# Performance work log

Hardware: AMD Instinct MI355X
Metric: run time of the kernel (lower is better)

The kernel has to match this reference:

```python
import jax, jax.numpy as jnp
import numpy as np

NEG = -1.0e9  # large negative number used for causal masking in the original


def setup_inputs() -> dict:
    key = jax.random.key(0)
    ks = jax.random.split(key, 9)
    B, S, D, H = 4, 4096, 512, 64
    sd = 1.0 / np.sqrt(D)
    sh = 1.0 / np.sqrt(H)
    return {
        "x": jax.random.normal(ks[0], (B, S, D), jnp.float32),
        # nn.Linear(d_model, d_head): stored here as (in, out) matrices
        "Wq": jax.random.normal(ks[1], (D, H), jnp.float32) * sd,
        "bq": jax.random.normal(ks[2], (H,), jnp.float32) * 0.01,
        "Wk": jax.random.normal(ks[3], (D, H), jnp.float32) * sd,
        "bk": jax.random.normal(ks[4], (H,), jnp.float32) * 0.01,
        "Wv": jax.random.normal(ks[5], (D, H), jnp.float32) * sd,
        "bv": jax.random.normal(ks[6], (H,), jnp.float32) * 0.01,
        "Wo": jax.random.normal(ks[7], (H, D), jnp.float32) * sh,
        "bo": jax.random.normal(ks[8], (D,), jnp.float32) * 0.01,
    }


def reference(x, Wq, bq, Wk, bk, Wv, bv, Wo, bo):
    # x: (B, S, D)
    B, S, D = x.shape
    Q = x @ Wq + bq  # (B, S, H)
    K = x @ Wk + bk
    V = x @ Wv + bv
    scores = jnp.einsum("bsh,bth->bst", Q, K)  # (B, S, S)
    # NOTE: original divides by sqrt(scores.shape[-1]) == sqrt(seq_len), not sqrt(d_head)
    scores = scores / jnp.sqrt(jnp.asarray(S, scores.dtype))
    # causal mask: strictly-upper-triangular entries get NEG added
    mask = jnp.triu(jnp.full((S, S), NEG, dtype=scores.dtype), k=1)
    attn = jax.nn.softmax(scores + mask[None, :, :], axis=-1)
    out = jnp.einsum("bst,bth->bsh", attn, V)  # (B, S, H)
    return out @ Wo + bo  # (B, S, D)
```

## Files before the change

### kernel.cpp

```cpp
#include <hip/hip_runtime.h>

#define S_LEN 4096
#define NROWS 16384

typedef __attribute__((ext_vector_type(8))) __bf16 bf16x8;
typedef __attribute__((ext_vector_type(8))) unsigned short ushort8;
typedef __attribute__((ext_vector_type(4))) float floatx4;

__device__ __forceinline__ unsigned short f2bf(float f) {
    unsigned int u = __float_as_uint(f);
    unsigned int r = (u + 0x7fffu + ((u >> 16) & 1u)) >> 16;
    return (unsigned short)r;
}

__device__ __forceinline__ float fexp2(float x) {
#if __has_builtin(__builtin_amdgcn_exp2f)
    return __builtin_amdgcn_exp2f(x);
#else
    float r; asm("v_exp_f32 %0, %1" : "=v"(r) : "v"(x)); return r;
#endif
}

__device__ __forceinline__ bf16x8 cvt_bf16x8(float4 a, float4 b) {
    union { ushort8 u; bf16x8 v; } r;
    r.u[0] = f2bf(a.x); r.u[1] = f2bf(a.y); r.u[2] = f2bf(a.z); r.u[3] = f2bf(a.w);
    r.u[4] = f2bf(b.x); r.u[5] = f2bf(b.y); r.u[6] = f2bf(b.z); r.u[7] = f2bf(b.w);
    return r.v;
}

__global__ __launch_bounds__(256) void convw_kernel(
    const float* __restrict__ Wq, const float* __restrict__ Wk,
    const float* __restrict__ Wv, const float* __restrict__ Wo,
    unsigned short* __restrict__ WqT, unsigned short* __restrict__ WkT,
    unsigned short* __restrict__ WvT, unsigned short* __restrict__ WoT)
{
    int tid = blockIdx.x * 256 + threadIdx.x;
    int n = tid >> 9, k = tid & 511;
    WqT[tid] = f2bf(Wq[k * 64 + n]);
    WkT[tid] = f2bf(Wk[k * 64 + n]);
    WvT[tid] = f2bf(Wv[k * 64 + n]);
    int n2 = tid >> 6, k2 = tid & 63;
    WoT[tid] = f2bf(Wo[k2 * 512 + n2]);
}

__global__ __launch_bounds__(192) void qkv_kernel(
    const float* __restrict__ x,
    const unsigned short* __restrict__ WqT, const unsigned short* __restrict__ WkT,
    const unsigned short* __restrict__ WvT,
    const float* __restrict__ bq, const float* __restrict__ bk, const float* __restrict__ bv,
    unsigned short* __restrict__ Qb, unsigned short* __restrict__ KF,
    unsigned short* __restrict__ VF)
{
    const int row0 = blockIdx.x * 16;
    const int tid = threadIdx.x;
    const int m = tid >> 6;
    const int lane = tid & 63, cl = lane & 15, quad = lane >> 4;
    const unsigned short* WT = (m == 0) ? WqT : (m == 1) ? WkT : WvT;
    const float* bias = (m == 0) ? bq : (m == 1) ? bk : bv;

    floatx4 acc[4];
    #pragma unroll
    for (int t = 0; t < 4; t++) acc[t] = (floatx4){0.f, 0.f, 0.f, 0.f};
    const float* xrow = x + (size_t)(row0 + cl) * 512;
    #pragma unroll 2
    for (int kc = 0; kc < 16; kc++) {
        const int k0 = kc * 32 + quad * 8;
        float4 xa = *(const float4*)(xrow + k0);
        float4 xb = *(const float4*)(xrow + k0 + 4);
        bf16x8 af = cvt_bf16x8(xa, xb);
        #pragma unroll
        for (int t = 0; t < 4; t++) {
            bf16x8 bf = *(const bf16x8*)(const void*)(WT + (t * 16 + cl) * 512 + k0);
            acc[t] = __builtin_amdgcn_mfma_f32_16x16x32_bf16(af, bf, acc[t], 0, 0, 0);
        }
    }
    if (m == 0) {
        const float scl = 0.022542110013890054f;
        #pragma unroll
        for (int t = 0; t < 4; t++) {
            const int d = t * 16 + cl;
            const float bd = bias[d];
            #pragma unroll
            for (int r = 0; r < 4; r++)
                Qb[(size_t)(row0 + quad * 4 + r) * 64 + d] = f2bf((acc[t][r] + bd) * scl);
        }
    } else if (m == 1) {
        const int g16 = row0 >> 4;
        #pragma unroll
        for (int t = 0; t < 4; t++) {
            const int d = t * 16 + cl;
            const float bd = bias[d];
            const size_t base = ((size_t)g16 * 8 + (d >> 3)) * 128 + (d & 7);
            #pragma unroll
            for (int r = 0; r < 4; r++)
                KF[base + (quad * 4 + r) * 8] = f2bf(acc[t][r] + bd);
        }
    } else {
        const int b = row0 >> 12, s_base = row0 & 4095;
        #pragma unroll
        for (int t = 0; t < 4; t++) {
            const int d = t * 16 + cl;
            const float bd = bias[d];
            #pragma unroll
            for (int r = 0; r < 4; r++) {
                const int s = s_base + quad * 4 + r;
                const size_t off = (size_t)b * (S_LEN * 64) + (size_t)(s >> 6) * 4096
                                 + ((s >> 5) & 1) * 2048 + t * 512 + cl * 32
                                 + ((s >> 3) & 3) * 8 + (s & 7);
                VF[off] = f2bf(acc[t][r] + bd);
            }
        }
    }
}

#define PSTR 152
__global__ __launch_bounds__(256, 2) void attn_kernel(
    const unsigned short* __restrict__ Qb, const unsigned short* __restrict__ Kb,
    const unsigned short* __restrict__ Vt,
    float* __restrict__ Po, float* __restrict__ Pl)
{
    __shared__ float4 shraw[4][304];
    const int bid = blockIdx.x;
    const int pair = bid >> 2, h = bid & 3;
    const int a = 63 - (pair >> 2);
    const int b = pair & 3;
    const int q0 = a * 64;
    const int nkt = a + 1;
    const int kt0 = (h * nkt) >> 2;
    const int kt1 = ((h + 1) * nkt) >> 2;
    const int tid = threadIdx.x;
    const int w = tid >> 6, lane = tid & 63, cl = lane & 15, quad = lane >> 4;

    const size_t qrow = (size_t)b * S_LEN + q0 + w * 16 + cl;
    const bf16x8 aq0 = *(const bf16x8*)(const void*)(Qb + qrow * 64 + quad * 8);
    const bf16x8 aq1 = *(const bf16x8*)(const void*)(Qb + qrow * 64 + 32 + quad * 8);
    const unsigned short* kbb = Kb + (size_t)b * S_LEN * 64;
    const unsigned short* vbb = Vt + (size_t)b * S_LEN * 64;
    const int qm = q0 + w * 16 + quad * 4;

    float lrow[4];
    floatx4 Oacc[4];
    #pragma unroll
    for (int r = 0; r < 4; r++) lrow[r] = 0.f;
    #pragma unroll
    for (int u = 0; u < 4; u++) Oacc[u] = (floatx4){0.f, 0.f, 0.f, 0.f};

    unsigned short* Pw = (unsigned short*)&shraw[w][0];

    int jt = kt0;
    for (; jt + 1 < kt1; jt += 2) {
        __syncthreads();
        float z[8][4];
        bf16x8 vf[8][2];
        {
            bf16x8 kf[4][2];
            #pragma unroll
            for (int t = 0; t < 4; t++) {
                const unsigned short* kp = kbb + ((size_t)(jt * 4 + t) * 8 + quad) * 128 + cl * 8;
                kf[t][0] = *(const bf16x8*)(const void*)kp;
                kf[t][1] = *(const bf16x8*)(const void*)(kp + 512);
            }
            #pragma unroll
            for (int t = 0; t < 4; t++) {
                floatx4 acc = (floatx4){0.f, 0.f, 0.f, 0.f};
                acc = __builtin_amdgcn_mfma_f32_16x16x32_bf16(aq0, kf[t][0], acc, 0, 0, 0);
                acc = __builtin_amdgcn_mfma_f32_16x16x32_bf16(aq1, kf[t][1], acc, 0, 0, 0);
                #pragma unroll
                for (int r = 0; r < 4; r++) z[t][r] = acc[r];
            }
        }
        #pragma unroll
        for (int u = 0; u < 4; u++) {
            const unsigned short* vp = vbb + (size_t)jt * 4096 + u * 512 + cl * 32 + quad * 8;
            vf[u][0] = *(const bf16x8*)(const void*)vp;
            vf[u][1] = *(const bf16x8*)(const void*)(vp + 2048);
        }
        {
            bf16x8 kf[4][2];
            #pragma unroll
            for (int t = 0; t < 4; t++) {
                const unsigned short* kp = kbb + ((size_t)((jt + 1) * 4 + t) * 8 + quad) * 128 + cl * 8;
                kf[t][0] = *(const bf16x8*)(const void*)kp;
                kf[t][1] = *(const bf16x8*)(const void*)(kp + 512);
            }
            #pragma unroll
            for (int t = 0; t < 4; t++) {
                floatx4 acc = (floatx4){0.f, 0.f, 0.f, 0.f};
                acc = __builtin_amdgcn_mfma_f32_16x16x32_bf16(aq0, kf[t][0], acc, 0, 0, 0);
                acc = __builtin_amdgcn_mfma_f32_16x16x32_bf16(aq1, kf[t][1], acc, 0, 0, 0);
                #pragma unroll
                for (int r = 0; r < 4; r++) z[4 + t][r] = acc[r];
            }
        }
        #pragma unroll
        for (int u = 0; u < 4; u++) {
            const unsigned short* vp = vbb + (size_t)(jt + 1) * 4096 + u * 512 + cl * 32 + quad * 8;
            vf[4 + u][0] = *(const bf16x8*)(const void*)vp;
            vf[4 + u][1] = *(const bf16x8*)(const void*)(vp + 2048);
        }
        if (jt + 1 == nkt - 1) {
            const int j0b = (jt + 1) * 64;
            #pragma unroll
            for (int t = 0; t < 4; t++)
                #pragma unroll
                for (int r = 0; r < 4; r++)
                    if (j0b + t * 16 + cl > qm + r) z[4 + t][r] = -1e30f;
        }
        #pragma unroll
        for (int t = 0; t < 8; t++)
            #pragma unroll
            for (int r = 0; r < 4; r++) z[t][r] = fexp2(z[t][r]);
        #pragma unroll
        for (int r = 0; r < 4; r++)
            lrow[r] += ((z[0][r] + z[1][r]) + (z[2][r] + z[3][r]))
                     + ((z[4][r] + z[5][r]) + (z[6][r] + z[7][r]));
        #pragma unroll
        for (int t = 0; t < 8; t++)
            #pragma unroll
            for (int r = 0; r < 4; r++)
                Pw[(quad * 4 + r) * PSTR + t * 16 + cl] = f2bf(z[t][r]);
        bf16x8 ap0 = *(const bf16x8*)(const void*)(Pw + cl * PSTR + quad * 8);
        bf16x8 ap1 = *(const bf16x8*)(const void*)(Pw + cl * PSTR + 32 + quad * 8);
        bf16x8 ap2 = *(const bf16x8*)(const void*)(Pw + cl * PSTR + 64 + quad * 8);
        bf16x8 ap3 = *(const bf16x8*)(const void*)(Pw + cl * PSTR + 96 + quad * 8);
        #pragma unroll
        for (int u = 0; u < 4; u++) {
            Oacc[u] = __builtin_amdgcn_mfma_f32_16x16x32_bf16(ap0, vf[u][0], Oacc[u], 0, 0, 0);
            Oacc[u] = __builtin_amdgcn_mfma_f32_16x16x32_bf16(ap1, vf[u][1], Oacc[u], 0, 0, 0);
            Oacc[u] = __builtin_amdgcn_mfma_f32_16x16x32_bf16(ap2, vf[4 + u][0], Oacc[u], 0, 0, 0);
            Oacc[u] = __builtin_amdgcn_mfma_f32_16x16x32_bf16(ap3, vf[4 + u][1], Oacc[u], 0, 0, 0);
        }
    }
    if (jt < kt1) {
        bf16x8 kf[4][2], vf[4][2];
        #pragma unroll
        for (int t = 0; t < 4; t++) {
            const unsigned short* kp = kbb + ((size_t)(jt * 4 + t) * 8 + quad) * 128 + cl * 8;
            kf[t][0] = *(const bf16x8*)(const void*)kp;
            kf[t][1] = *(const bf16x8*)(const void*)(kp + 512);
        }
        #pragma unroll
        for (int u = 0; u < 4; u++) {
            const unsigned short* vp = vbb + (size_t)jt * 4096 + u * 512 + cl * 32 + quad * 8;
            vf[u][0] = *(const bf16x8*)(const void*)vp;
            vf[u][1] = *(const bf16x8*)(const void*)(vp + 2048);
        }
        float z[4][4];
        #pragma unroll
        for (int t = 0; t < 4; t++) {
            floatx4 acc = (floatx4){0.f, 0.f, 0.f, 0.f};
            acc = __builtin_amdgcn_mfma_f32_16x16x32_bf16(aq0, kf[t][0], acc, 0, 0, 0);
            acc = __builtin_amdgcn_mfma_f32_16x16x32_bf16(aq1, kf[t][1], acc, 0, 0, 0);
            #pragma unroll
            for (int r = 0; r < 4; r++) z[t][r] = acc[r];
        }
        if (jt == nkt - 1) {
            const int j0 = jt * 64;
            #pragma unroll
            for (int t = 0; t < 4; t++)
                #pragma unroll
                for (int r = 0; r < 4; r++)
                    if (j0 + t * 16 + cl > qm + r) z[t][r] = -1e30f;
        }
        #pragma unroll
        for (int t = 0; t < 4; t++)
            #pragma unroll
            for (int r = 0; r < 4; r++) z[t][r] = fexp2(z[t][r]);
        #pragma unroll
        for (int r = 0; r < 4; r++)
            lrow[r] += ((z[0][r] + z[1][r]) + (z[2][r] + z[3][r]));
        #pragma unroll
        for (int t = 0; t < 4; t++)
            #pragma unroll
            for (int r = 0; r < 4; r++)
                Pw[(quad * 4 + r) * PSTR + t * 16 + cl] = f2bf(z[t][r]);
        bf16x8 ap0 = *(const bf16x8*)(const void*)(Pw + cl * PSTR + quad * 8);
        bf16x8 ap1 = *(const bf16x8*)(const void*)(Pw + cl * PSTR + 32 + quad * 8);
        #pragma unroll
        for (int u = 0; u < 4; u++) {
            Oacc[u] = __builtin_amdgcn_mfma_f32_16x16x32_bf16(ap0, vf[u][0], Oacc[u], 0, 0, 0);
            Oacc[u] = __builtin_amdgcn_mfma_f32_16x16x32_bf16(ap1, vf[u][1], Oacc[u], 0, 0, 0);
        }
    }
    #pragma unroll
    for (int r = 0; r < 4; r++) {
        float s = lrow[r];
        s += __shfl_xor(s, 1, 64);
        s += __shfl_xor(s, 2, 64);
        s += __shfl_xor(s, 4, 64);
        s += __shfl_xor(s, 8, 64);
        lrow[r] = s;
    }
    {
        float* pob = Po + (size_t)bid * 64 * 64;
        #pragma unroll
        for (int u = 0; u < 4; u++)
            #pragma unroll
            for (int r = 0; r < 4; r++)
                pob[(size_t)(w * 16 + quad * 4 + r) * 64 + u * 16 + cl] = Oacc[u][r];
        if (cl == 0) {
            #pragma unroll
            for (int r = 0; r < 4; r++)
                Pl[(size_t)bid * 64 + w * 16 + quad * 4 + r] = lrow[r];
        }
    }
}

__global__ __launch_bounds__(256) void amerge_kernel(
    const float* __restrict__ Po, const float* __restrict__ Pl,
    unsigned short* __restrict__ Ob)
{
    const int pair = blockIdx.x;
    const int a = 63 - (pair >> 2), b = pair & 3;
    const int tid = threadIdx.x;
    const int d0 = (tid & 15) * 4, r0 = tid >> 4;
    const size_t base = (size_t)pair * 4;
    #pragma unroll
    for (int rr = 0; rr < 4; rr++) {
        const int row = r0 + rr * 16;
        const float L = Pl[(base + 0) * 64 + row] + Pl[(base + 1) * 64 + row]
                      + Pl[(base + 2) * 64 + row] + Pl[(base + 3) * 64 + row];
        const float invL = 1.0f / L;
        const float4 a0 = *(const float4*)(Po + ((base + 0) * 64 + row) * 64 + d0);
        const float4 a1 = *(const float4*)(Po + ((base + 1) * 64 + row) * 64 + d0);
        const float4 a2 = *(const float4*)(Po + ((base + 2) * 64 + row) * 64 + d0);
        const float4 a3 = *(const float4*)(Po + ((base + 3) * 64 + row) * 64 + d0);
        unsigned short ov[4];
        ov[0] = f2bf((a0.x + a1.x + a2.x + a3.x) * invL);
        ov[1] = f2bf((a0.y + a1.y + a2.y + a3.y) * invL);
        ov[2] = f2bf((a0.z + a1.z + a2.z + a3.z) * invL);
        ov[3] = f2bf((a0.w + a1.w + a2.w + a3.w) * invL);
        *(uint2*)(void*)(Ob + ((size_t)b * S_LEN + a * 64 + row) * 64 + d0) = *(const uint2*)ov;
    }
}

__global__ __launch_bounds__(256) void oproj_kernel(
    const unsigned short* __restrict__ Ob, const unsigned short* __restrict__ WoT,
    const float* __restrict__ bo, float* __restrict__ out)
{
    const int row0 = blockIdx.x * 16;
    const int tid = threadIdx.x;
    const int w = tid >> 6, lane = tid & 63, cl = lane & 15, quad = lane >> 4;
    const unsigned short* op = Ob + (size_t)(row0 + cl) * 64 + quad * 8;
    const bf16x8 a0 = *(const bf16x8*)(const void*)op;
    const bf16x8 a1 = *(const bf16x8*)(const void*)(op + 32);
    #pragma unroll 2
    for (int i = 0; i < 8; i++) {
        const int n = w * 128 + i * 16 + cl;
        const unsigned short* wp = WoT + (size_t)n * 64 + quad * 8;
        bf16x8 b0 = *(const bf16x8*)(const void*)wp;
        bf16x8 b1 = *(const bf16x8*)(const void*)(wp + 32);
        floatx4 acc = (floatx4){0.f, 0.f, 0.f, 0.f};
        acc = __builtin_amdgcn_mfma_f32_16x16x32_bf16(a0, b0, acc, 0, 0, 0);
        acc = __builtin_amdgcn_mfma_f32_16x16x32_bf16(a1, b1, acc, 0, 0, 0);
        const float bod = bo[n];
        #pragma unroll
        for (int r = 0; r < 4; r++)
            out[(size_t)(row0 + quad * 4 + r) * 512 + n] = acc[r] + bod;
    }
}

extern "C" void kernel_launch(void* const* d_in, const int* in_sizes, int n_in,
                              void* d_out, int out_size, void* d_ws, size_t ws_size,
                              hipStream_t stream) {
    const float* x  = (const float*)d_in[0];
    const float* Wq = (const float*)d_in[1];
    const float* bq = (const float*)d_in[2];
    const float* Wk = (const float*)d_in[3];
    const float* bk = (const float*)d_in[4];
    const float* Wv = (const float*)d_in[5];
    const float* bv = (const float*)d_in[6];
    const float* Wo = (const float*)d_in[7];
    const float* bo = (const float*)d_in[8];
    float* out = (float*)d_out;

    unsigned short* Qb  = (unsigned short*)d_ws;
    unsigned short* KF  = Qb + (size_t)NROWS * 64;
    unsigned short* VF  = KF + (size_t)NROWS * 64;
    unsigned short* Ob  = VF + (size_t)NROWS * 64;
    unsigned short* WqT = Ob + (size_t)NROWS * 64;
    unsigned short* WkT = WqT + 512 * 64;
    unsigned short* WvT = WkT + 512 * 64;
    unsigned short* WoT = WvT + 512 * 64;
    float* Pl = (float*)(WoT + 512 * 64);
    float* Po = out;

    convw_kernel<<<128, 256, 0, stream>>>(Wq, Wk, Wv, Wo, WqT, WkT, WvT, WoT);
    qkv_kernel<<<1024, 192, 0, stream>>>(x, WqT, WkT, WvT, bq, bk, bv, Qb, KF, VF);
    attn_kernel<<<1024, 256, 0, stream>>>(Qb, KF, VF, Po, Pl);
    amerge_kernel<<<256, 256, 0, stream>>>(Po, Pl, Ob);
    oproj_kernel<<<NROWS / 16, 256, 0, stream>>>(Ob, WoT, bo, out);
}
```

Before: 172.3 us.

## Store weights and attention output in MFMA fragment order; stage x in LDS

Weights and the merged attention output are now written in a fragment-major layout, so each lane's 8-element MFMA operand is one contiguous, coalesced 16-byte load. The QKV kernel converts the 16-row x tile to bf16 once into shared memory in fragment order, so the three waves share it instead of each reloading and converting from global memory. This adds an LDS staging pass and a block barrier in the QKV kernel.

```diff
diff --git a/kernel.cpp b/kernel.cpp
--- a/kernel.cpp
+++ b/kernel.cpp
@@ -5,6 +5,7 @@
 
 typedef __attribute__((ext_vector_type(8))) __bf16 bf16x8;
 typedef __attribute__((ext_vector_type(8))) unsigned short ushort8;
+typedef __attribute__((ext_vector_type(4))) unsigned short ushort4_t;
 typedef __attribute__((ext_vector_type(4))) float floatx4;
 
 __device__ __forceinline__ unsigned short f2bf(float f) {
@@ -21,56 +22,65 @@
 #endif
 }
 
-__device__ __forceinline__ bf16x8 cvt_bf16x8(float4 a, float4 b) {
-    union { ushort8 u; bf16x8 v; } r;
-    r.u[0] = f2bf(a.x); r.u[1] = f2bf(a.y); r.u[2] = f2bf(a.z); r.u[3] = f2bf(a.w);
-    r.u[4] = f2bf(b.x); r.u[5] = f2bf(b.y); r.u[6] = f2bf(b.z); r.u[7] = f2bf(b.w);
-    return r.v;
-}
-
 __global__ __launch_bounds__(256) void convw_kernel(
     const float* __restrict__ Wq, const float* __restrict__ Wk,
     const float* __restrict__ Wv, const float* __restrict__ Wo,
-    unsigned short* __restrict__ WqT, unsigned short* __restrict__ WkT,
-    unsigned short* __restrict__ WvT, unsigned short* __restrict__ WoT)
+    unsigned short* __restrict__ WqF, unsigned short* __restrict__ WkF,
+    unsigned short* __restrict__ WvF, unsigned short* __restrict__ WoF)
 {
     int tid = blockIdx.x * 256 + threadIdx.x;
-    int n = tid >> 9, k = tid & 511;
-    WqT[tid] = f2bf(Wq[k * 64 + n]);
-    WkT[tid] = f2bf(Wk[k * 64 + n]);
-    WvT[tid] = f2bf(Wv[k * 64 + n]);
-    int n2 = tid >> 6, k2 = tid & 63;
-    WoT[tid] = f2bf(Wo[k2 * 512 + n2]);
+    {
+        const int e = tid & 7, cl = (tid >> 3) & 15, quad = (tid >> 7) & 3;
+        const int kc = (tid >> 9) & 15, t = tid >> 13;
+        const int n = t * 16 + cl, k = kc * 32 + quad * 8 + e;
+        WqF[tid] = f2bf(Wq[k * 64 + n]);
+        WkF[tid] = f2bf(Wk[k * 64 + n]);
+        WvF[tid] = f2bf(Wv[k * 64 + n]);
+    }
+    {
+        const int e = tid & 7, cl = (tid >> 3) & 15, quad = (tid >> 7) & 3;
+        const int h = (tid >> 9) & 1, g = tid >> 10;
+        const int n = g * 16 + cl, k = h * 32 + quad * 8 + e;
+        WoF[tid] = f2bf(Wo[k * 512 + n]);
+    }
 }
 
 __global__ __launch_bounds__(192) void qkv_kernel(
     const float* __restrict__ x,
-    const unsigned short* __restrict__ WqT, const unsigned short* __restrict__ WkT,
-    const unsigned short* __restrict__ WvT,
+    const unsigned short* __restrict__ WqF, const unsigned short* __restrict__ WkF,
+    const unsigned short* __restrict__ WvF,
     const float* __restrict__ bq, const float* __restrict__ bk, const float* __restrict__ bv,
     unsigned short* __restrict__ Qb, unsigned short* __restrict__ KF,
     unsigned short* __restrict__ VF)
 {
+    __shared__ unsigned short xs[8192];
     const int row0 = blockIdx.x * 16;
     const int tid = threadIdx.x;
+
+    const float* xt = x + (size_t)row0 * 512;
+    for (int i = tid; i < 2048; i += 192) {
+        float4 v = *(const float4*)(xt + i * 4);
+        const int r = i >> 7, k = (i & 127) * 4;
+        ushort4_t o;
+        o[0] = f2bf(v.x); o[1] = f2bf(v.y); o[2] = f2bf(v.z); o[3] = f2bf(v.w);
+        *(ushort4_t*)(xs + (k >> 5) * 512 + ((k >> 3) & 3) * 128 + r * 8 + (k & 7)) = o;
+    }
+    __syncthreads();
+
     const int m = tid >> 6;
     const int lane = tid & 63, cl = lane & 15, quad = lane >> 4;
-    const unsigned short* WT = (m == 0) ? WqT : (m == 1) ? WkT : WvT;
+    const unsigned short* WF = (m == 0) ? WqF : (m == 1) ? WkF : WvF;
     const float* bias = (m == 0) ? bq : (m == 1) ? bk : bv;
 
     floatx4 acc[4];
     #pragma unroll
     for (int t = 0; t < 4; t++) acc[t] = (floatx4){0.f, 0.f, 0.f, 0.f};
-    const float* xrow = x + (size_t)(row0 + cl) * 512;
     #pragma unroll 2
     for (int kc = 0; kc < 16; kc++) {
-        const int k0 = kc * 32 + quad * 8;
-        float4 xa = *(const float4*)(xrow + k0);
-        float4 xb = *(const float4*)(xrow + k0 + 4);
-        bf16x8 af = cvt_bf16x8(xa, xb);
-        #pragma unroll
-        for (int t = 0; t < 4; t++) {
-            bf16x8 bf = *(const bf16x8*)(const void*)(WT + (t * 16 + cl) * 512 + k0);
+        const bf16x8 af = *(const bf16x8*)(const void*)(xs + kc * 512 + lane * 8);
+        #pragma unroll
+        for (int t = 0; t < 4; t++) {
+            const bf16x8 bf = *(const bf16x8*)(const void*)(WF + (size_t)(t * 16 + kc) * 512 + lane * 8);
             acc[t] = __builtin_amdgcn_mfma_f32_16x16x32_bf16(af, bf, acc[t], 0, 0, 0);
         }
     }
@@ -308,13 +318,14 @@
 
 __global__ __launch_bounds__(256) void amerge_kernel(
     const float* __restrict__ Po, const float* __restrict__ Pl,
-    unsigned short* __restrict__ Ob)
+    unsigned short* __restrict__ ObF)
 {
     const int pair = blockIdx.x;
     const int a = 63 - (pair >> 2), b = pair & 3;
     const int tid = threadIdx.x;
     const int d0 = (tid & 15) * 4, r0 = tid >> 4;
     const size_t base = (size_t)pair * 4;
+    const int h2 = d0 >> 5, qd = (d0 >> 3) & 3, e0 = d0 & 7;
     #pragma unroll
     for (int rr = 0; rr < 4; rr++) {
         const int row = r0 + rr * 16;
@@ -325,31 +336,33 @@
         const float4 a1 = *(const float4*)(Po + ((base + 1) * 64 + row) * 64 + d0);
         const float4 a2 = *(const float4*)(Po + ((base + 2) * 64 + row) * 64 + d0);
         const float4 a3 = *(const float4*)(Po + ((base + 3) * 64 + row) * 64 + d0);
-        unsigned short ov[4];
+        ushort4_t ov;
         ov[0] = f2bf((a0.x + a1.x + a2.x + a3.x) * invL);
         ov[1] = f2bf((a0.y + a1.y + a2.y + a3.y) * invL);
         ov[2] = f2bf((a0.z + a1.z + a2.z + a3.z) * invL);
         ov[3] = f2bf((a0.w + a1.w + a2.w + a3.w) * invL);
-        *(uint2*)(void*)(Ob + ((size_t)b * S_LEN + a * 64 + row) * 64 + d0) = *(const uint2*)ov;
+        const int blk16 = b * 256 + a * 4 + (row >> 4);
+        const size_t idx = (size_t)(blk16 * 2 + h2) * 512 + (qd * 16 + (row & 15)) * 8 + e0;
+        *(ushort4_t*)(ObF + idx) = ov;
     }
 }
 
 __global__ __launch_bounds__(256) void oproj_kernel(
-    const unsigned short* __restrict__ Ob, const unsigned short* __restrict__ WoT,
+    const unsigned short* __restrict__ ObF, const unsigned short* __restrict__ WoF,
     const float* __restrict__ bo, float* __restrict__ out)
 {
-    const int row0 = blockIdx.x * 16;
+    const int blk = blockIdx.x;
+    const int row0 = blk * 16;
     const int tid = threadIdx.x;
     const int w = tid >> 6, lane = tid & 63, cl = lane & 15, quad = lane >> 4;
-    const unsigned short* op = Ob + (size_t)(row0 + cl) * 64 + quad * 8;
-    const bf16x8 a0 = *(const bf16x8*)(const void*)op;
-    const bf16x8 a1 = *(const bf16x8*)(const void*)(op + 32);
+    const bf16x8 a0 = *(const bf16x8*)(const void*)(ObF + (size_t)(blk * 2 + 0) * 512 + lane * 8);
+    const bf16x8 a1 = *(const bf16x8*)(const void*)(ObF + (size_t)(blk * 2 + 1) * 512 + lane * 8);
     #pragma unroll 2
     for (int i = 0; i < 8; i++) {
-        const int n = w * 128 + i * 16 + cl;
-        const unsigned short* wp = WoT + (size_t)n * 64 + quad * 8;
-        bf16x8 b0 = *(const bf16x8*)(const void*)wp;
-        bf16x8 b1 = *(const bf16x8*)(const void*)(wp + 32);
+        const int g = w * 8 + i;
+        const int n = g * 16 + cl;
+        bf16x8 b0 = *(const bf16x8*)(const void*)(WoF + (size_t)(g * 2 + 0) * 512 + lane * 8);
+        bf16x8 b1 = *(const bf16x8*)(const void*)(WoF + (size_t)(g * 2 + 1) * 512 + lane * 8);
         floatx4 acc = (floatx4){0.f, 0.f, 0.f, 0.f};
         acc = __builtin_amdgcn_mfma_f32_16x16x32_bf16(a0, b0, acc, 0, 0, 0);
         acc = __builtin_amdgcn_mfma_f32_16x16x32_bf16(a1, b1, acc, 0, 0, 0);
@@ -377,17 +390,17 @@
     unsigned short* Qb  = (unsigned short*)d_ws;
     unsigned short* KF  = Qb + (size_t)NROWS * 64;
     unsigned short* VF  = KF + (size_t)NROWS * 64;
-    unsigned short* Ob  = VF + (size_t)NROWS * 64;
-    unsigned short* WqT = Ob + (size_t)NROWS * 64;
-    unsigned short* WkT = WqT + 512 * 64;
-    unsigned short* WvT = WkT + 512 * 64;
-    unsigned short* WoT = WvT + 512 * 64;
-    float* Pl = (float*)(WoT + 512 * 64);
+    unsigned short* ObF = VF + (size_t)NROWS * 64;
+    unsigned short* WqF = ObF + (size_t)NROWS * 64;
+    unsigned short* WkF = WqF + 512 * 64;
+    unsigned short* WvF = WkF + 512 * 64;
+    unsigned short* WoF = WvF + 512 * 64;
+    float* Pl = (float*)(WoF + 512 * 64);
     float* Po = out;
 
-    convw_kernel<<<128, 256, 0, stream>>>(Wq, Wk, Wv, Wo, WqT, WkT, WvT, WoT);
-    qkv_kernel<<<1024, 192, 0, stream>>>(x, WqT, WkT, WvT, bq, bk, bv, Qb, KF, VF);
+    convw_kernel<<<128, 256, 0, stream>>>(Wq, Wk, Wv, Wo, WqF, WkF, WvF, WoF);
+    qkv_kernel<<<1024, 192, 0, stream>>>(x, WqF, WkF, WvF, bq, bk, bv, Qb, KF, VF);
     attn_kernel<<<1024, 256, 0, stream>>>(Qb, KF, VF, Po, Pl);
-    amerge_kernel<<<256, 256, 0, stream>>>(Po, Pl, Ob);
-    oproj_kernel<<<NROWS / 16, 256, 0, stream>>>(Ob, WoT, bo, out);
-}
+    amerge_kernel<<<256, 256, 0, stream>>>(Po, Pl, ObF);
+    oproj_kernel<<<NROWS / 16, 256, 0, stream>>>(ObF, WoF, bo, out);
+}
```

New measurement: 151.4 us. 12.2% less time.
